# Kernel optimization log

Measured on AMD Instinct MI355X. Metric: run time of the kernel, lower is better.

Reference implementation:

```python
import jax, jax.numpy as jnp
import numpy as np

N_NODES = 100000   # number of nodes
N_EDGES = 20000    # number of hyperedges
N_INC = 800000     # incidence (node, hyperedge) pairs
TEXT_DIM = 384     # all-MiniLM-L6-v2 sentence embedding dim
HID = 128          # hidden_dim in _init_model


def setup_inputs() -> dict:
    key = jax.random.key(0)
    ks = jax.random.split(key, 16)
    s = 1.0 / np.sqrt(HID)
    inp = {
        "text_emb": jax.random.normal(ks[0], (N_NODES, TEXT_DIM), jnp.float32),
        "W_proj": jax.random.normal(ks[1], (TEXT_DIM, HID), jnp.float32) / np.sqrt(TEXT_DIM),
        "b_proj": jnp.zeros((HID,), jnp.float32),
        # weight generator 0 (Linear-ReLU-Dropout(eval)-Linear)
        "W1a": jax.random.normal(ks[2], (HID, HID), jnp.float32) * s,
        "b1a": jnp.zeros((HID,), jnp.float32),
        "W2a": jax.random.normal(ks[3], (HID, HID), jnp.float32) * s,
        "b2a": jnp.zeros((HID,), jnp.float32),
        # weight generator 1
        "W1b": jax.random.normal(ks[4], (HID, HID), jnp.float32) * s,
        "b1b": jnp.zeros((HID,), jnp.float32),
        "W2b": jax.random.normal(ks[5], (HID, HID), jnp.float32) * s,
        "b2b": jnp.zeros((HID,), jnp.float32),
        "node_idx": jax.random.randint(ks[6], (N_INC,), 0, N_NODES),
        "edge_idx": jax.random.randint(ks[7], (N_INC,), 0, N_EDGES),
    }
    return inp


def _segment_mean(vals, idx, num_segments):
    # vals: [E_inc, D]; idx: [E_inc] -> [num_segments, D]
    ssum = jax.ops.segment_sum(vals, idx, num_segments=num_segments)
    cnt = jax.ops.segment_sum(jnp.ones((idx.shape[0], 1), vals.dtype), idx,
                              num_segments=num_segments)
    return ssum / jnp.maximum(cnt, 1.0)


def reference(text_emb, W_proj, b_proj,
              W1a, b1a, W2a, b2a,
              W1b, b1b, W2b, b2b,
              node_idx, edge_idx):
    # text projection to hidden space: [N, 128]
    h = text_emb @ W_proj + b_proj
    gens = ((W1a, b1a, W2a, b2a), (W1b, b1b, W2b, b2b))
    for (W1, b1, W2, b2) in gens:  # 2 hypergraph layers (fixed by code)
        # hypernetwork: generate per-layer dynamic modulation from pooled context
        g = jnp.mean(h, axis=0)                               # [128]
        scale = jnp.maximum(g @ W1 + b1, 0.0) @ W2 + b2       # [128]
        # gather node -> hyperedge, aggregate (mean) per hyperedge
        e_feat = _segment_mean(h[node_idx], edge_idx, N_EDGES)   # [E, 128]
        # gather hyperedge -> node, aggregate (mean) per node (scatter)
        m = _segment_mean(e_feat[edge_idx], node_idx, N_NODES)   # [N, 128]
        h = jax.nn.relu(m * scale)
    return h
```

## Files before the change

### kernel.cpp

```cpp
#include <hip/hip_runtime.h>

#define N_NODES 100000
#define N_EDGES 20000
#define N_INC   800000
#define TDIM    384
#define HID     128
#define NOFF    800000
#define EPAD    8
#define NPAD    4

#define PROJ_BLOCKS 1563
#define CNT_BLOCKS  512
#define FILLE_BLOCKS 1024
#define FILLN_BLOCKS 1024
#define EAGG_BLOCKS 5000
#define NAGG_BLOCKS 2500

typedef __attribute__((ext_vector_type(8))) short short8;
typedef __attribute__((ext_vector_type(4))) float floatx4;

static __device__ __forceinline__ unsigned short f32_bf16_rne(float f) {
  unsigned int u = __float_as_uint(f);
  unsigned int r = u + 0x7FFFu + ((u >> 16) & 1u);
  return (unsigned short)(r >> 16);
}

__global__ __launch_bounds__(64) void wprep_kernel(
    const float* __restrict__ W, unsigned short* __restrict__ Bh,
    unsigned short* __restrict__ Bl)
{
  int b = blockIdx.x;
  int lane = threadIdx.x;
  int kk = b >> 3, nt = b & 7;
  int col = lane & 15, quad = lane >> 4;
  size_t o = ((size_t)b * 64 + lane) * 8;
#pragma unroll
  for (int j = 0; j < 8; ++j) {
    int k = kk * 32 + quad * 8 + j;
    float w = W[(size_t)k * HID + nt * 16 + col];
    unsigned short h = f32_bf16_rne(w);
    float hf = __uint_as_float((unsigned int)h << 16);
    Bh[o + j] = h;
    Bl[o + j] = f32_bf16_rne(w - hf);
  }
}

__global__ __launch_bounds__(256) void proj_count_kernel(
    const float* __restrict__ A, const unsigned short* __restrict__ Bh,
    const unsigned short* __restrict__ Bl, const float* __restrict__ bias,
    unsigned short* __restrict__ Hb, float* __restrict__ gsum0,
    const int* __restrict__ node_idx, const int* __restrict__ edge_idx,
    int* __restrict__ ecp, int* __restrict__ ncp)
{
  __shared__ unsigned short BhS[512 * 8];
  __shared__ unsigned short BlS[512 * 8];
  __shared__ float red[4][HID];
  const int tid = threadIdx.x;

  if (blockIdx.x >= PROJ_BLOCKS) {
    int start = (blockIdx.x - PROJ_BLOCKS) * 256 + tid;
    for (int i = start; i < N_INC; i += CNT_BLOCKS * 256) {
      int ed = edge_idx[i];
      int nd = node_idx[i];
      atomicAdd(&ecp[ed * EPAD], 1);
      atomicAdd(&ncp[nd * NPAD], 1);
    }
    return;
  }

  const int wave = tid >> 6;
  const int lane = tid & 63;
  const int col = lane & 15;
  const int quad = lane >> 4;
  const int m0 = blockIdx.x * 64 + wave * 16;

  floatx4 acc[8];
#pragma unroll
  for (int nt = 0; nt < 8; ++nt) acc[nt] = (floatx4){0.f, 0.f, 0.f, 0.f};

  int r = m0 + col;
  if (r >= N_NODES) r = N_NODES - 1;
  const float* arow = A + (size_t)r * TDIM + quad * 8;

  float ra[8];
  *(float4*)(&ra[0]) = *(const float4*)(arow);
  *(float4*)(&ra[4]) = *(const float4*)(arow + 4);

  for (int kk = 0; kk < 12; ++kk) {
    short8 sh0 = *(const short8*)(Bh + ((size_t)kk * 512 + tid) * 8);
    short8 sh1 = *(const short8*)(Bh + ((size_t)kk * 512 + tid + 256) * 8);
    short8 sl0 = *(const short8*)(Bl + ((size_t)kk * 512 + tid) * 8);
    short8 sl1 = *(const short8*)(Bl + ((size_t)kk * 512 + tid + 256) * 8);
    __syncthreads();
    *(short8*)(BhS + (size_t)tid * 8) = sh0;
    *(short8*)(BhS + ((size_t)tid + 256) * 8) = sh1;
    *(short8*)(BlS + (size_t)tid * 8) = sl0;
    *(short8*)(BlS + ((size_t)tid + 256) * 8) = sl1;

    float rn[8];
    if (kk < 11) {
      *(float4*)(&rn[0]) = *(const float4*)(arow + (kk + 1) * 32);
      *(float4*)(&rn[4]) = *(const float4*)(arow + (kk + 1) * 32 + 4);
    }

    short8 ah, al;
#pragma unroll
    for (int j = 0; j < 8; ++j) {
      float f = ra[j];
      unsigned short h = f32_bf16_rne(f);
      float hf = __uint_as_float((unsigned int)h << 16);
      ah[j] = (short)h;
      al[j] = (short)f32_bf16_rne(f - hf);
    }
    __syncthreads();

#pragma unroll
    for (int nt = 0; nt < 8; ++nt) {
      short8 bh = *(const short8*)(BhS + ((size_t)nt * 64 + lane) * 8);
      short8 bl = *(const short8*)(BlS + ((size_t)nt * 64 + lane) * 8);
      acc[nt] = __builtin_amdgcn_mfma_f32_16x16x32_bf16(ah, bh, acc[nt], 0, 0, 0);
      acc[nt] = __builtin_amdgcn_mfma_f32_16x16x32_bf16(al, bh, acc[nt], 0, 0, 0);
      acc[nt] = __builtin_amdgcn_mfma_f32_16x16x32_bf16(ah, bl, acc[nt], 0, 0, 0);
    }
#pragma unroll
    for (int j = 0; j < 8; ++j) ra[j] = rn[j];
  }

#pragma unroll
  for (int nt = 0; nt < 8; ++nt) {
    float bv = bias[nt * 16 + col];
    float p = 0.f;
#pragma unroll
    for (int rr = 0; rr < 4; ++rr) {
      int row = m0 + quad * 4 + rr;
      float v = acc[nt][rr] + bv;
      if (row < N_NODES) {
        Hb[(size_t)row * HID + nt * 16 + col] = f32_bf16_rne(v);
        p += v;
      }
    }
    p += __shfl_xor(p, 16, 64);
    p += __shfl_xor(p, 32, 64);
    if (quad == 0) red[wave][nt * 16 + col] = p;
  }
  __syncthreads();
  if (tid < HID) {
    float a = red[0][tid] + red[1][tid] + red[2][tid] + red[3][tid];
    atomicAdd(&gsum0[(blockIdx.x & 7) * HID + tid], a);
  }
}

static __device__ __forceinline__ int padded_cnt(const int* ecp, const int* ncp, int i) {
  return (i < N_EDGES) ? ecp[i * EPAD] : ncp[(i - N_EDGES) * NPAD];
}

__global__ __launch_bounds__(1024) void scan_block(const int* __restrict__ ecp,
                                                   const int* __restrict__ ncp,
                                                   int* __restrict__ ptr,
                                                   int* __restrict__ partials, int n)
{
  __shared__ int s[1024];
  int tid = threadIdx.x;
  int i = blockIdx.x * 1024 + tid;
  int v = (i < n) ? padded_cnt(ecp, ncp, i) : 0;
  s[tid] = v;
  __syncthreads();
  for (int off = 1; off < 1024; off <<= 1) {
    int add = (tid >= off) ? s[tid - off] : 0;
    __syncthreads();
    s[tid] += add;
    __syncthreads();
  }
  if (i < n) ptr[i] = s[tid] - v;
  if (tid == 1023) partials[blockIdx.x] = s[1023];
}

__global__ __launch_bounds__(1024) void scan_partials(int* __restrict__ partials, int nb,
                                                      int* __restrict__ ptr, int n)
{
  __shared__ int s[1024];
  int tid = threadIdx.x;
  int v = (tid < nb) ? partials[tid] : 0;
  s[tid] = v;
  __syncthreads();
  for (int off = 1; off < 1024; off <<= 1) {
    int add = (tid >= off) ? s[tid - off] : 0;
    __syncthreads();
    s[tid] += add;
    __syncthreads();
  }
  if (tid < nb) partials[tid] = s[tid] - v;
  if (tid == 0) ptr[n] = s[1023];
}

__global__ void scan_add(int* __restrict__ ptr, const int* __restrict__ partials,
                         int* __restrict__ ecp, int* __restrict__ ncp, int n)
{
  int i = blockIdx.x * 1024 + threadIdx.x;
  if (i >= n) return;
  int v = ptr[i] + partials[blockIdx.x];
  ptr[i] = v;
  if (i < N_EDGES) ecp[i * EPAD] = v;
  else ncp[(i - N_EDGES) * NPAD] = v - NOFF;
}

__global__ __launch_bounds__(256) void fill_kernel(
    const int* __restrict__ node_idx, const int* __restrict__ edge_idx,
    int* __restrict__ ecp, int* __restrict__ ncp,
    int* __restrict__ ecols, int* __restrict__ ncols)
{
  int bid = blockIdx.x;
  int tid = threadIdx.x;
  if (bid < FILLE_BLOCKS) {
    for (int i = bid * 256 + tid; i < N_INC; i += FILLE_BLOCKS * 256) {
      int ed = edge_idx[i];
      int nd = node_idx[i];
      int p = atomicAdd(&ecp[ed * EPAD], 1);
      ecols[p] = nd;
    }
  } else {
    bid -= FILLE_BLOCKS;
    for (int i = bid * 256 + tid; i < N_INC; i += FILLN_BLOCKS * 256) {
      int ed = edge_idx[i];
      int nd = node_idx[i];
      int q = atomicAdd(&ncp[nd * NPAD], 1);
      ncols[q] = ed;
    }
  }
}

__global__ __launch_bounds__(256) void edge_agg_scale_kernel(
    const unsigned short* __restrict__ Hb, const int* __restrict__ eptr,
    const int* __restrict__ ecols, unsigned short* __restrict__ Eb,
    const float* __restrict__ gsum,
    const float* __restrict__ W1, const float* __restrict__ b1,
    const float* __restrict__ W2, const float* __restrict__ b2,
    float* __restrict__ scale)
{
  if (blockIdx.x >= EAGG_BLOCKS) {
    __shared__ float g[HID], t[HID];
    int c = threadIdx.x;
    if (c < HID) {
      float s = 0.f;
#pragma unroll
      for (int k = 0; k < 8; ++k) s += gsum[k * HID + c];
      g[c] = s * (1.0f / (float)N_NODES);
    }
    __syncthreads();
    if (c < HID) {
      float acc = b1[c];
#pragma unroll 8
      for (int k = 0; k < HID; ++k) acc += g[k] * W1[(size_t)k * HID + c];
      t[c] = fmaxf(acc, 0.f);
    }
    __syncthreads();
    if (c < HID) {
      float acc2 = b2[c];
#pragma unroll 8
      for (int k = 0; k < HID; ++k) acc2 += t[k] * W2[(size_t)k * HID + c];
      scale[c] = acc2;
    }
    return;
  }
  int gw = blockIdx.x * 4 + (threadIdx.x >> 6);
  int lane = threadIdx.x & 63;
  int p0 = eptr[gw], p1 = eptr[gw + 1];
  float ax0 = 0.f, ay0 = 0.f, ax1 = 0.f, ay1 = 0.f;
  float ax2 = 0.f, ay2 = 0.f, ax3 = 0.f, ay3 = 0.f;
  for (int base = p0; base < p1; base += 64) {
    int cnt = min(64, p1 - base);
    int idx = (base + lane < p1) ? ecols[base + lane] : 0;
    int j = 0;
    for (; j + 3 < cnt; j += 4) {
      int n0 = __shfl(idx, j, 64);
      int n1 = __shfl(idx, j + 1, 64);
      int n2 = __shfl(idx, j + 2, 64);
      int n3 = __shfl(idx, j + 3, 64);
      unsigned v0 = *(const unsigned*)(Hb + (size_t)n0 * HID + lane * 2);
      unsigned v1 = *(const unsigned*)(Hb + (size_t)n1 * HID + lane * 2);
      unsigned v2 = *(const unsigned*)(Hb + (size_t)n2 * HID + lane * 2);
      unsigned v3 = *(const unsigned*)(Hb + (size_t)n3 * HID + lane * 2);
      ax0 += __uint_as_float(v0 << 16); ay0 += __uint_as_float(v0 & 0xffff0000u);
      ax1 += __uint_as_float(v1 << 16); ay1 += __uint_as_float(v1 & 0xffff0000u);
      ax2 += __uint_as_float(v2 << 16); ay2 += __uint_as_float(v2 & 0xffff0000u);
      ax3 += __uint_as_float(v3 << 16); ay3 += __uint_as_float(v3 & 0xffff0000u);
    }
    for (; j < cnt; ++j) {
      int n0 = __shfl(idx, j, 64);
      unsigned v0 = *(const unsigned*)(Hb + (size_t)n0 * HID + lane * 2);
      ax0 += __uint_as_float(v0 << 16); ay0 += __uint_as_float(v0 & 0xffff0000u);
    }
  }
  float inv = 1.f / (float)max(p1 - p0, 1);
  float sx = ((ax0 + ax1) + (ax2 + ax3)) * inv;
  float sy = ((ay0 + ay1) + (ay2 + ay3)) * inv;
  unsigned pk = ((unsigned)f32_bf16_rne(sy) << 16) | f32_bf16_rne(sx);
  *(unsigned*)(Eb + (size_t)gw * HID + lane * 2) = pk;
}

__global__ __launch_bounds__(256) void node_agg_kernel(
    const unsigned short* __restrict__ Eb, const int* __restrict__ nptr,
    const int* __restrict__ ncols, const float* __restrict__ scale,
    unsigned short* __restrict__ Hb, float* __restrict__ H,
    float* __restrict__ gsum, int do_aux)
{
  __shared__ float red[4][HID];
  int wave = threadIdx.x >> 6, lane = threadIdx.x & 63;
  float2 sc = *(const float2*)(scale + lane * 2);
  float csx = 0.f, csy = 0.f;
  for (int gw = blockIdx.x * 4 + wave; gw < N_NODES; gw += NAGG_BLOCKS * 4) {
    int p0 = nptr[gw] - NOFF, p1 = nptr[gw + 1] - NOFF;
    float ax0 = 0.f, ay0 = 0.f, ax1 = 0.f, ay1 = 0.f;
    float ax2 = 0.f, ay2 = 0.f, ax3 = 0.f, ay3 = 0.f;
    for (int base = p0; base < p1; base += 64) {
      int cnt = min(64, p1 - base);
      int idx = (base + lane < p1) ? ncols[base + lane] : 0;
      int j = 0;
      for (; j + 3 < cnt; j += 4) {
        int e0 = __shfl(idx, j, 64);
        int e1 = __shfl(idx, j + 1, 64);
        int e2 = __shfl(idx, j + 2, 64);
        int e3 = __shfl(idx, j + 3, 64);
        unsigned v0 = *(const unsigned*)(Eb + (size_t)e0 * HID + lane * 2);
        unsigned v1 = *(const unsigned*)(Eb + (size_t)e1 * HID + lane * 2);
        unsigned v2 = *(const unsigned*)(Eb + (size_t)e2 * HID + lane * 2);
        unsigned v3 = *(const unsigned*)(Eb + (size_t)e3 * HID + lane * 2);
        ax0 += __uint_as_float(v0 << 16); ay0 += __uint_as_float(v0 & 0xffff0000u);
        ax1 += __uint_as_float(v1 << 16); ay1 += __uint_as_float(v1 & 0xffff0000u);
        ax2 += __uint_as_float(v2 << 16); ay2 += __uint_as_float(v2 & 0xffff0000u);
        ax3 += __uint_as_float(v3 << 16); ay3 += __uint_as_float(v3 & 0xffff0000u);
      }
      for (; j < cnt; ++j) {
        int e0 = __shfl(idx, j, 64);
        unsigned v0 = *(const unsigned*)(Eb + (size_t)e0 * HID + lane * 2);
        ax0 += __uint_as_float(v0 << 16); ay0 += __uint_as_float(v0 & 0xffff0000u);
      }
    }
    float inv = 1.f / (float)max(p1 - p0, 1);
    float ox = fmaxf(((ax0 + ax1) + (ax2 + ax3)) * inv * sc.x, 0.f);
    float oy = fmaxf(((ay0 + ay1) + (ay2 + ay3)) * inv * sc.y, 0.f);
    if (do_aux) {
      unsigned pk = ((unsigned)f32_bf16_rne(oy) << 16) | f32_bf16_rne(ox);
      *(unsigned*)(Hb + (size_t)gw * HID + lane * 2) = pk;
      csx += ox; csy += oy;
    } else {
      *(float2*)(H + (size_t)gw * HID + lane * 2) = make_float2(ox, oy);
    }
  }
  if (do_aux) {
    red[wave][lane * 2] = csx;
    red[wave][lane * 2 + 1] = csy;
    __syncthreads();
    if (threadIdx.x < HID) {
      int c = threadIdx.x;
      float a = red[0][c] + red[1][c] + red[2][c] + red[3][c];
      atomicAdd(&gsum[(blockIdx.x & 7) * HID + c], a);
    }
  }
}

extern "C" void kernel_launch(void* const* d_in, const int* in_sizes, int n_in,
                              void* d_out, int out_size, void* d_ws, size_t ws_size,
                              hipStream_t stream)
{
  const float* text = (const float*)d_in[0];
  const float* Wp   = (const float*)d_in[1];
  const float* bp   = (const float*)d_in[2];
  const float* W1a  = (const float*)d_in[3];
  const float* b1a  = (const float*)d_in[4];
  const float* W2a  = (const float*)d_in[5];
  const float* b2a  = (const float*)d_in[6];
  const float* W1b  = (const float*)d_in[7];
  const float* b1b  = (const float*)d_in[8];
  const float* W2b  = (const float*)d_in[9];
  const float* b2b  = (const float*)d_in[10];
  const int* node_idx = (const int*)d_in[11];
  const int* edge_idx = (const int*)d_in[12];
  float* H = (float*)d_out;

  char* ws = (char*)d_ws;
  int*   ecp   = (int*)(ws + 0);
  int*   ncp   = (int*)(ws + 640000);
  float* gsum0 = (float*)(ws + 2240000);
  float* gsum1 = (float*)(ws + 2244096);
  const size_t zero_bytes = 2248192;
  int*   cptr  = (int*)(ws + 2248192);
  int*   eptr  = cptr;
  int*   nptr  = cptr + N_EDGES;
  int*   ecols = (int*)(ws + 2728208);
  int*   ncols = (int*)(ws + 5928208);
  float* scale0 = (float*)(ws + 9128208);
  float* scale1 = (float*)(ws + 9128720);
  int*   partials = (int*)(ws + 9129232);
  unsigned short* Eb = (unsigned short*)(ws + 9133328);
  unsigned short* Hb = (unsigned short*)(ws + 14253328);
  unsigned short* Bh = (unsigned short*)(ws + 2728208);
  unsigned short* Bl = (unsigned short*)(ws + 2826512);

  hipMemsetAsync(ws, 0, zero_bytes, stream);

  wprep_kernel<<<96, 64, 0, stream>>>(Wp, Bh, Bl);
  proj_count_kernel<<<PROJ_BLOCKS + CNT_BLOCKS, 256, 0, stream>>>(
      text, Bh, Bl, bp, Hb, gsum0, node_idx, edge_idx, ecp, ncp);

  scan_block<<<118, 1024, 0, stream>>>(ecp, ncp, cptr, partials, 120000);
  scan_partials<<<1, 1024, 0, stream>>>(partials, 118, cptr, 120000);
  scan_add<<<118, 1024, 0, stream>>>(cptr, partials, ecp, ncp, 120000);

  fill_kernel<<<FILLE_BLOCKS + FILLN_BLOCKS, 256, 0, stream>>>(
      node_idx, edge_idx, ecp, ncp, ecols, ncols);

  edge_agg_scale_kernel<<<EAGG_BLOCKS + 1, 256, 0, stream>>>(
      Hb, eptr, ecols, Eb, gsum0, W1a, b1a, W2a, b2a, scale0);
  node_agg_kernel<<<NAGG_BLOCKS, 256, 0, stream>>>(
      Eb, nptr, ncols, scale0, Hb, H, gsum1, 1);

  edge_agg_scale_kernel<<<EAGG_BLOCKS + 1, 256, 0, stream>>>(
      Hb, eptr, ecols, Eb, gsum1, W1b, b1b, W2b, b2b, scale1);
  node_agg_kernel<<<NAGG_BLOCKS, 256, 0, stream>>>(
      Eb, nptr, ncols, scale1, Hb, H, gsum1, 0);
}
```

Measured before the change: 651.0 us.

## Record atomic ranks during counting to make CSR fill atomic-free

Result: faster. 558.1 us (-14.3%).

```diff
diff --git a/kernel.cpp b/kernel.cpp
--- a/kernel.cpp
+++ b/kernel.cpp
@@ -11,8 +11,7 @@
 
 #define PROJ_BLOCKS 1563
 #define CNT_BLOCKS  512
-#define FILLE_BLOCKS 1024
-#define FILLN_BLOCKS 1024
+#define FILL_BLOCKS 3125
 #define EAGG_BLOCKS 5000
 #define NAGG_BLOCKS 2500
 
@@ -50,7 +49,8 @@
     const unsigned short* __restrict__ Bl, const float* __restrict__ bias,
     unsigned short* __restrict__ Hb, float* __restrict__ gsum0,
     const int* __restrict__ node_idx, const int* __restrict__ edge_idx,
-    int* __restrict__ ecp, int* __restrict__ ncp)
+    int* __restrict__ ecp, int* __restrict__ ncp,
+    int* __restrict__ rank_e, int* __restrict__ rank_n)
 {
   __shared__ unsigned short BhS[512 * 8];
   __shared__ unsigned short BlS[512 * 8];
@@ -62,8 +62,8 @@
     for (int i = start; i < N_INC; i += CNT_BLOCKS * 256) {
       int ed = edge_idx[i];
       int nd = node_idx[i];
-      atomicAdd(&ecp[ed * EPAD], 1);
-      atomicAdd(&ncp[nd * NPAD], 1);
+      rank_e[i] = atomicAdd(&ecp[ed * EPAD], 1);
+      rank_n[i] = atomicAdd(&ncp[nd * NPAD], 1);
     }
     return;
   }
@@ -193,40 +193,26 @@
   if (tid == 0) ptr[n] = s[1023];
 }
 
-__global__ void scan_add(int* __restrict__ ptr, const int* __restrict__ partials,
-                         int* __restrict__ ecp, int* __restrict__ ncp, int n)
+__global__ void scan_add(int* __restrict__ ptr, const int* __restrict__ partials, int n)
 {
   int i = blockIdx.x * 1024 + threadIdx.x;
   if (i >= n) return;
-  int v = ptr[i] + partials[blockIdx.x];
-  ptr[i] = v;
-  if (i < N_EDGES) ecp[i * EPAD] = v;
-  else ncp[(i - N_EDGES) * NPAD] = v - NOFF;
+  ptr[i] += partials[blockIdx.x];
 }
 
 __global__ __launch_bounds__(256) void fill_kernel(
     const int* __restrict__ node_idx, const int* __restrict__ edge_idx,
-    int* __restrict__ ecp, int* __restrict__ ncp,
+    const int* __restrict__ rank_e, const int* __restrict__ rank_n,
+    const int* __restrict__ eptr, const int* __restrict__ nptr,
     int* __restrict__ ecols, int* __restrict__ ncols)
 {
-  int bid = blockIdx.x;
-  int tid = threadIdx.x;
-  if (bid < FILLE_BLOCKS) {
-    for (int i = bid * 256 + tid; i < N_INC; i += FILLE_BLOCKS * 256) {
-      int ed = edge_idx[i];
-      int nd = node_idx[i];
-      int p = atomicAdd(&ecp[ed * EPAD], 1);
-      ecols[p] = nd;
-    }
-  } else {
-    bid -= FILLE_BLOCKS;
-    for (int i = bid * 256 + tid; i < N_INC; i += FILLN_BLOCKS * 256) {
-      int ed = edge_idx[i];
-      int nd = node_idx[i];
-      int q = atomicAdd(&ncp[nd * NPAD], 1);
-      ncols[q] = ed;
-    }
-  }
+  int i = blockIdx.x * 256 + threadIdx.x;
+  int ed = edge_idx[i];
+  int nd = node_idx[i];
+  int p = eptr[ed] + rank_e[i];
+  int q = nptr[nd] - NOFF + rank_n[i];
+  __builtin_nontemporal_store(nd, &ecols[p]);
+  __builtin_nontemporal_store(ed, &ncols[q]);
 }
 
 __global__ __launch_bounds__(256) void edge_agg_scale_kernel(
@@ -396,19 +382,21 @@
   unsigned short* Hb = (unsigned short*)(ws + 14253328);
   unsigned short* Bh = (unsigned short*)(ws + 2728208);
   unsigned short* Bl = (unsigned short*)(ws + 2826512);
+  int*   rank_e = (int*)d_out;
+  int*   rank_n = rank_e + N_INC;
 
   hipMemsetAsync(ws, 0, zero_bytes, stream);
 
   wprep_kernel<<<96, 64, 0, stream>>>(Wp, Bh, Bl);
   proj_count_kernel<<<PROJ_BLOCKS + CNT_BLOCKS, 256, 0, stream>>>(
-      text, Bh, Bl, bp, Hb, gsum0, node_idx, edge_idx, ecp, ncp);
+      text, Bh, Bl, bp, Hb, gsum0, node_idx, edge_idx, ecp, ncp, rank_e, rank_n);
 
   scan_block<<<118, 1024, 0, stream>>>(ecp, ncp, cptr, partials, 120000);
   scan_partials<<<1, 1024, 0, stream>>>(partials, 118, cptr, 120000);
-  scan_add<<<118, 1024, 0, stream>>>(cptr, partials, ecp, ncp, 120000);
-
-  fill_kernel<<<FILLE_BLOCKS + FILLN_BLOCKS, 256, 0, stream>>>(
-      node_idx, edge_idx, ecp, ncp, ecols, ncols);
+  scan_add<<<118, 1024, 0, stream>>>(cptr, partials, 120000);
+
+  fill_kernel<<<FILL_BLOCKS, 256, 0, stream>>>(
+      node_idx, edge_idx, rank_e, rank_n, eptr, nptr, ecols, ncols);
 
   edge_agg_scale_kernel<<<EAGG_BLOCKS + 1, 256, 0, stream>>>(
       Hb, eptr, ecols, Eb, gsum0, W1a, b1a, W2a, b2a, scale0);
```
